# Kernel tuning notes

Hardware: AMD Instinct MI355X
Metric: run time of the kernel (lower is better)

The kernel has to match this reference:

```python
import jax, jax.numpy as jnp
import numpy as np

N_NODES = 100000
N_EDGES = 1600000
NODE_DIM = 128
EDGE_DIM = 32
HIDDEN_DIM = 256


def _linear_params(key, fan_in, fan_out):
    kw, kb = jax.random.split(key)
    bound = 1.0 / np.sqrt(fan_in)
    W = jax.random.uniform(kw, (fan_in, fan_out), minval=-bound, maxval=bound, dtype=jnp.float32)
    b = jax.random.uniform(kb, (fan_out,), minval=-bound, maxval=bound, dtype=jnp.float32)
    return W, b


def setup_inputs() -> dict:
    key = jax.random.key(0)
    ks = jax.random.split(key, 8)
    x = jax.random.normal(ks[0], (N_NODES, NODE_DIM), dtype=jnp.float32)
    edge_index = jax.random.randint(ks[1], (2, N_EDGES), 0, N_NODES, dtype=jnp.int64)
    edge_attr = jax.random.normal(ks[2], (N_EDGES, EDGE_DIM), dtype=jnp.float32)
    congestion = jax.random.uniform(ks[3], (N_NODES,), dtype=jnp.float32)
    msg_in = 2 * NODE_DIM + EDGE_DIM + 1
    mW1, mb1 = _linear_params(ks[4], msg_in, HIDDEN_DIM)
    mW2, mb2 = _linear_params(ks[5], HIDDEN_DIM, NODE_DIM)
    uW1, ub1 = _linear_params(ks[6], 2 * NODE_DIM, HIDDEN_DIM)
    uW2, ub2 = _linear_params(ks[7], HIDDEN_DIM, NODE_DIM)
    return {
        "x": x, "edge_index": edge_index, "edge_attr": edge_attr, "congestion": congestion,
        "mW1": mW1, "mb1": mb1, "mW2": mW2, "mb2": mb2,
        "uW1": uW1, "ub1": ub1, "uW2": uW2, "ub2": ub2,
    }


def reference(x, edge_index, edge_attr, congestion, mW1, mb1, mW2, mb2, uW1, ub1, uW2, ub2):
    src, dst = edge_index[0], edge_index[1]
    # gather node features and src congestion, concat along feature dim  [E, 2D+edge_dim+1]
    msg_in = jnp.concatenate(
        [x[src], x[dst], edge_attr, congestion[src][:, None]], axis=-1)
    h = jax.nn.relu(msg_in @ mW1 + mb1)          # [E, hidden]
    messages = h @ mW2 + mb2                     # [E, node_dim]
    # scatter_add messages into destination nodes  [N, node_dim]
    aggregated = jax.ops.segment_sum(messages, dst, num_segments=x.shape[0])
    upd_in = jnp.concatenate([x, aggregated], axis=-1)  # [N, 2*node_dim]
    h2 = jax.nn.relu(upd_in @ uW1 + ub1)
    x_new = h2 @ uW2 + ub2                       # [N, node_dim]
    return x_new
```

## Files before the change

### kernel.cpp

```cpp
#include <hip/hip_runtime.h>

#define E_TOTAL 1600000
#define NN 100000
#define D 128
#define ED 32
#define H 256

typedef __attribute__((ext_vector_type(8))) short s16x8;
typedef __attribute__((ext_vector_type(4))) short s16x4;
typedef __attribute__((ext_vector_type(4))) float f32x4;

#define MFMA(a, b, c) __builtin_amdgcn_mfma_f32_16x16x32_bf16((a), (b), (c), 0, 0, 0)

__device__ __forceinline__ short f2bf(float f) {
    unsigned u = __builtin_bit_cast(unsigned, f);
    u += 0x7fffu + ((u >> 16) & 1u);
    return (short)(u >> 16);
}

__device__ __forceinline__ void gll16(const void* g, void* l) {
    __builtin_amdgcn_global_load_lds(
        (const __attribute__((address_space(1))) void*)g,
        (__attribute__((address_space(3))) void*)l, 16, 0, 0);
}

__global__ void k_cvt_x(const float* __restrict__ x, short* __restrict__ xb, int n) {
    int i = (blockIdx.x * blockDim.x + threadIdx.x) * 4;
    if (i >= n) return;
    f32x4 v = *(const f32x4*)(x + i);
    s16x4 o;
    o[0] = f2bf(v[0]); o[1] = f2bf(v[1]); o[2] = f2bf(v[2]); o[3] = f2bf(v[3]);
    *(s16x4*)(xb + i) = o;
}

__global__ void k_swz(const float* __restrict__ W, short* __restrict__ out,
                      int K, int N, int total) {
    int idx = blockIdx.x * blockDim.x + threadIdx.x;
    if (idx >= total) return;
    int j    = idx & 7;
    int lane = (idx >> 3) & 63;
    int rest = idx >> 9;
    int NT   = N >> 4;
    int nt   = rest % NT;
    int t    = rest / NT;
    int k    = t * 32 + (lane >> 4) * 8 + j;
    int col  = nt * 16 + (lane & 15);
    float v  = (k < K) ? W[k * N + col] : 0.f;
    out[idx] = f2bf(v);
}

__global__ void k_hist(const int* __restrict__ ei, int* __restrict__ cnt) {
    int e = blockIdx.x * blockDim.x + threadIdx.x;
    if (e >= E_TOTAL) return;
    atomicAdd(&cnt[ei[E_TOTAL + e]], 1);
}

__global__ void k_scan1(int* __restrict__ cnt, int* __restrict__ psum, int n) {
    __shared__ int wsum[16];
    __shared__ int woff[16];
    const int tid = threadIdx.x, lane = tid & 63, wv = tid >> 6;
    int i = blockIdx.x * 1024 + tid;
    int v = (i < n) ? cnt[i] : 0;
    int s = v;
#pragma unroll
    for (int off = 1; off < 64; off <<= 1) {
        int u = __shfl_up(s, off, 64);
        if (lane >= off) s += u;
    }
    if (lane == 63) wsum[wv] = s;
    __syncthreads();
    if (wv == 0 && lane < 16) {
        int t = wsum[lane];
        int sc = t;
#pragma unroll
        for (int off = 1; off < 16; off <<= 1) {
            int u = __shfl_up(sc, off, 16);
            if (lane >= off) sc += u;
        }
        woff[lane] = sc - t;
    }
    __syncthreads();
    int excl = (s - v) + woff[wv];
    if (i < n) cnt[i] = excl;
    if (tid == 1023) psum[blockIdx.x] = excl + v;
}

__global__ void k_scan2(int* __restrict__ psum, int nb) {
    __shared__ int w0;
    const int tid = threadIdx.x, lane = tid & 63, wv = tid >> 6;
    int v = (tid < nb) ? psum[tid] : 0;
    int s = v;
#pragma unroll
    for (int off = 1; off < 64; off <<= 1) {
        int u = __shfl_up(s, off, 64);
        if (lane >= off) s += u;
    }
    if (wv == 0 && lane == 63) w0 = s;
    __syncthreads();
    int excl = (s - v) + (wv ? w0 : 0);
    if (tid < nb) psum[tid] = excl;
}

__global__ void k_scan3(const int* __restrict__ psum, int* __restrict__ cnt, int n) {
    int i = blockIdx.x * 1024 + threadIdx.x;
    if (i < n) cnt[i] += psum[blockIdx.x];
}

__global__ void k_perm(const int* __restrict__ ei, int* __restrict__ cursor,
                       int* __restrict__ perm, int2* __restrict__ srcdst) {
    int e = blockIdx.x * blockDim.x + threadIdx.x;
    if (e >= E_TOTAL) return;
    int s = ei[e], d = ei[E_TOTAL + e];
    int pos = atomicAdd(&cursor[d], 1);
    perm[pos] = e;
    srcdst[pos] = make_int2(s, d);
}

__global__ __launch_bounds__(512, 4)
void k_edge(const short* __restrict__ xb, const int* __restrict__ perm,
            const int2* __restrict__ srcdst,
            const float* __restrict__ eattr, const float* __restrict__ cong,
            const short* __restrict__ W1s, const float* __restrict__ b1,
            const short* __restrict__ W2s, const float* __restrict__ b2,
            float* __restrict__ agg) {
    __shared__ char smem[73728];
    __shared__ int   dst_s[128];
    __shared__ short cong_s[128];

    const int tid  = threadIdx.x;
    const int lane = tid & 63;
    const int w    = tid >> 6;
    const int eh   = w >> 2;
    const int cg   = w & 3;
    const int m    = lane & 15;
    const int q    = lane >> 4;
    const int p0b  = blockIdx.x * 128;

    {
        int edge = w * 16 + (lane >> 2);
        int2 sd  = srcdst[p0b + edge];
        int kqs  = (lane & 3) ^ ((lane >> 3) & 3);
        const char* gx0 = (const char*)xb + (long)sd.x * 256 + kqs * 16;
        const char* gx1 = (const char*)xb + (long)sd.y * 256 + kqs * 16;
#pragma unroll
        for (int t = 0; t < 4; t++)
            gll16(gx0 + t * 64, smem + t * 8192 + w * 1024);
#pragma unroll
        for (int t = 0; t < 4; t++)
            gll16(gx1 + t * 64, smem + (4 + t) * 8192 + w * 1024);
        int ea = perm[p0b + edge];
        const float* ge = eattr + (long)ea * ED + kqs * 8;
        f32x4 e0 = *(const f32x4*)ge, e1 = *(const f32x4*)(ge + 4);
        s16x8 ev;
#pragma unroll
        for (int j = 0; j < 4; j++) { ev[j] = f2bf(e0[j]); ev[4 + j] = f2bf(e1[j]); }
        *(s16x8*)(smem + 8 * 8192 + w * 1024 + lane * 16) = ev;
        if (tid < 128) {
            int2 sd2 = srcdst[p0b + tid];
            dst_s[tid]  = sd2.y;
            cong_s[tid] = f2bf(cong[sd2.x]);
        }
    }
    __syncthreads();

    const int rdoff = m * 64 + ((q ^ ((m >> 1) & 3)) << 4);

    f32x4 acc[4][4];
#pragma unroll
    for (int mt = 0; mt < 4; mt++)
#pragma unroll
        for (int n = 0; n < 4; n++) acc[mt][n] = (f32x4){0.f, 0.f, 0.f, 0.f};

#pragma unroll
    for (int t = 0; t < 9; t++) {
        s16x8 b[4];
        const short* bw = W1s + (t * 16 + cg * 4) * 512 + lane * 8;
#pragma unroll
        for (int n = 0; n < 4; n++) b[n] = *(const s16x8*)(bw + n * 512);
#pragma unroll
        for (int mt = 0; mt < 4; mt++) {
            s16x8 a = *(const s16x8*)(smem + t * 8192 + (eh * 4 + mt) * 1024 + rdoff);
#pragma unroll
            for (int n = 0; n < 4; n++) acc[mt][n] = MFMA(a, b[n], acc[mt][n]);
        }
    }
    {
        s16x8 b[4];
        const short* bw = W1s + (9 * 16 + cg * 4) * 512 + lane * 8;
#pragma unroll
        for (int n = 0; n < 4; n++) b[n] = *(const s16x8*)(bw + n * 512);
#pragma unroll
        for (int mt = 0; mt < 4; mt++) {
            s16x8 a = (s16x8){0, 0, 0, 0, 0, 0, 0, 0};
            short cv = cong_s[eh * 64 + mt * 16 + m];
            a[0] = (q == 0) ? cv : (short)0;
#pragma unroll
            for (int n = 0; n < 4; n++) acc[mt][n] = MFMA(a, b[n], acc[mt][n]);
        }
    }
    __syncthreads();

    {
        short* hb16 = (short*)smem;
#pragma unroll
        for (int n = 0; n < 4; n++) {
            const int chunk = 2 * cg + (n >> 1);
            const int srq   = (n & 1) * 2 + (m >> 3);
            const float bias = b1[cg * 64 + n * 16 + m];
#pragma unroll
            for (int mt = 0; mt < 4; mt++) {
#pragma unroll
                for (int r = 0; r < 4; r++) {
                    int edge = eh * 64 + mt * 16 + q * 4 + r;
                    int key  = (2 * q + (r >> 1)) & 3;
                    int phys = srq ^ key;
                    float v  = acc[mt][n][r] + bias;
                    hb16[chunk * 4096 + edge * 32 + phys * 8 + (m & 7)] =
                        f2bf(v > 0.f ? v : 0.f);
                }
            }
        }
    }
    __syncthreads();

    f32x4 acc2[4][2];
#pragma unroll
    for (int mt = 0; mt < 4; mt++) {
        acc2[mt][0] = (f32x4){0.f, 0.f, 0.f, 0.f};
        acc2[mt][1] = (f32x4){0.f, 0.f, 0.f, 0.f};
    }
#pragma unroll
    for (int t2 = 0; t2 < 8; t2++) {
        const short* bw = W2s + (t2 * 8 + cg * 2) * 512 + lane * 8;
        s16x8 b0  = *(const s16x8*)bw;
        s16x8 b1v = *(const s16x8*)(bw + 512);
#pragma unroll
        for (int mt = 0; mt < 4; mt++) {
            s16x8 a = *(const s16x8*)(smem + t2 * 8192 + (eh * 4 + mt) * 1024 + rdoff);
            acc2[mt][0] = MFMA(a, b0, acc2[mt][0]);
            acc2[mt][1] = MFMA(a, b1v, acc2[mt][1]);
        }
    }
    __syncthreads();

    {
        float (*mbuf)[132] = (float (*)[132])smem;
        float bb0 = b2[cg * 32 + m];
        float bb1 = b2[cg * 32 + 16 + m];
#pragma unroll
        for (int mt = 0; mt < 4; mt++)
#pragma unroll
            for (int r = 0; r < 4; r++) {
                int edge = eh * 64 + mt * 16 + q * 4 + r;
                mbuf[edge][cg * 32 + m]      = acc2[mt][0][r] + bb0;
                mbuf[edge][cg * 32 + 16 + m] = acc2[mt][1][r] + bb1;
            }
    }
    __syncthreads();

    {
        float (*mbuf)[132] = (float (*)[132])smem;
        const int qtr = tid >> 7, cc = tid & 127;
        float s = 0.f;
        int prev = dst_s[qtr * 32];
        for (int row = qtr * 32; row < qtr * 32 + 32; row++) {
            int dcur = dst_s[row];
            if (dcur != prev) {
                __hip_atomic_fetch_add(agg + (long)prev * D + cc, s,
                                       __ATOMIC_RELAXED, __HIP_MEMORY_SCOPE_AGENT);
                s = 0.f; prev = dcur;
            }
            s += mbuf[row][cc];
        }
        __hip_atomic_fetch_add(agg + (long)prev * D + cc, s,
                               __ATOMIC_RELAXED, __HIP_MEMORY_SCOPE_AGENT);
    }
}

__global__ __launch_bounds__(512, 4)
void k_node(const short* __restrict__ xb, const float* __restrict__ agg,
            const short* __restrict__ U1s, const float* __restrict__ b1,
            const short* __restrict__ U2s, const float* __restrict__ b2,
            float* __restrict__ out) {
    __shared__ char smem[65536];
    const int tid  = threadIdx.x;
    const int lane = tid & 63;
    const int w    = tid >> 6;
    const int eh   = w >> 2;
    const int cg   = w & 3;
    const int m    = lane & 15;
    const int q    = lane >> 4;
    const int r0   = blockIdx.x * 128;

    {
        int rowl = w * 16 + (lane >> 2);
        int grow = r0 + rowl;
        int gc   = grow < NN ? grow : 0;
        int kqs  = (lane & 3) ^ ((lane >> 3) & 3);
        const char* gx = (const char*)xb + (long)gc * 256 + kqs * 16;
#pragma unroll
        for (int t = 0; t < 4; t++)
            gll16(gx + t * 64, smem + t * 8192 + w * 1024);
        const float* ga = agg + (long)gc * D + kqs * 8;
#pragma unroll
        for (int t = 0; t < 4; t++) {
            f32x4 a0 = *(const f32x4*)(ga + t * 32);
            f32x4 a1 = *(const f32x4*)(ga + t * 32 + 4);
            s16x8 v;
#pragma unroll
            for (int j = 0; j < 4; j++) { v[j] = f2bf(a0[j]); v[4 + j] = f2bf(a1[j]); }
            *(s16x8*)(smem + (4 + t) * 8192 + w * 1024 + lane * 16) = v;
        }
    }
    __syncthreads();

    const int rdoff = m * 64 + ((q ^ ((m >> 1) & 3)) << 4);

    f32x4 acc[4][4];
#pragma unroll
    for (int mt = 0; mt < 4; mt++)
#pragma unroll
        for (int n = 0; n < 4; n++) acc[mt][n] = (f32x4){0.f, 0.f, 0.f, 0.f};

#pragma unroll
    for (int t = 0; t < 8; t++) {
        s16x8 b[4];
        const short* bw = U1s + (t * 16 + cg * 4) * 512 + lane * 8;
#pragma unroll
        for (int n = 0; n < 4; n++) b[n] = *(const s16x8*)(bw + n * 512);
#pragma unroll
        for (int mt = 0; mt < 4; mt++) {
            s16x8 a = *(const s16x8*)(smem + t * 8192 + (eh * 4 + mt) * 1024 + rdoff);
#pragma unroll
            for (int n = 0; n < 4; n++) acc[mt][n] = MFMA(a, b[n], acc[mt][n]);
        }
    }
    __syncthreads();

    {
        short* hb16 = (short*)smem;
#pragma unroll
        for (int n = 0; n < 4; n++) {
            const int chunk = 2 * cg + (n >> 1);
            const int srq   = (n & 1) * 2 + (m >> 3);
            const float bias = b1[cg * 64 + n * 16 + m];
#pragma unroll
            for (int mt = 0; mt < 4; mt++) {
#pragma unroll
                for (int r = 0; r < 4; r++) {
                    int row = eh * 64 + mt * 16 + q * 4 + r;
                    int key = (2 * q + (r >> 1)) & 3;
                    int phys = srq ^ key;
                    float v = acc[mt][n][r] + bias;
                    hb16[chunk * 4096 + row * 32 + phys * 8 + (m & 7)] =
                        f2bf(v > 0.f ? v : 0.f);
                }
            }
        }
    }
    __syncthreads();

    f32x4 acc2[4][2];
#pragma unroll
    for (int mt = 0; mt < 4; mt++) {
        acc2[mt][0] = (f32x4){0.f, 0.f, 0.f, 0.f};
        acc2[mt][1] = (f32x4){0.f, 0.f, 0.f, 0.f};
    }
#pragma unroll
    for (int t2 = 0; t2 < 8; t2++) {
        const short* bw = U2s + (t2 * 8 + cg * 2) * 512 + lane * 8;
        s16x8 b0  = *(const s16x8*)bw;
        s16x8 b1v = *(const s16x8*)(bw + 512);
#pragma unroll
        for (int mt = 0; mt < 4; mt++) {
            s16x8 a = *(const s16x8*)(smem + t2 * 8192 + (eh * 4 + mt) * 1024 + rdoff);
            acc2[mt][0] = MFMA(a, b0, acc2[mt][0]);
            acc2[mt][1] = MFMA(a, b1v, acc2[mt][1]);
        }
    }

    {
        float bb0 = b2[cg * 32 + m];
        float bb1 = b2[cg * 32 + 16 + m];
#pragma unroll
        for (int mt = 0; mt < 4; mt++)
#pragma unroll
            for (int r = 0; r < 4; r++) {
                int grow = r0 + eh * 64 + mt * 16 + q * 4 + r;
                if (grow < NN) {
                    out[(long)grow * D + cg * 32 + m]      = acc2[mt][0][r] + bb0;
                    out[(long)grow * D + cg * 32 + 16 + m] = acc2[mt][1][r] + bb1;
                }
            }
    }
}

extern "C" void kernel_launch(void* const* d_in, const int* in_sizes, int n_in,
                              void* d_out, int out_size, void* d_ws, size_t ws_size,
                              hipStream_t stream) {
    const float* x     = (const float*)d_in[0];
    const int*   ei    = (const int*)d_in[1];
    const float* eattr = (const float*)d_in[2];
    const float* cong  = (const float*)d_in[3];
    const float* mW1   = (const float*)d_in[4];
    const float* mb1   = (const float*)d_in[5];
    const float* mW2   = (const float*)d_in[6];
    const float* mb2   = (const float*)d_in[7];
    const float* uW1   = (const float*)d_in[8];
    const float* ub1   = (const float*)d_in[9];
    const float* uW2   = (const float*)d_in[10];
    const float* ub2   = (const float*)d_in[11];

    char* ws = (char*)d_ws;
    float* agg    = (float*)ws;
    short* xb     = (short*)(ws + 51200000);
    short* W1s    = (short*)(ws + 76800000);
    short* W2s    = (short*)(ws + 76963840);
    short* U1s    = (short*)(ws + 77029376);
    short* U2s    = (short*)(ws + 77160448);
    int*   cnt    = (int*)(ws + 77225984);
    int*   perm   = (int*)(ws + 77625984);
    int2*  srcdst = (int2*)(ws + 84025984);
    int*   psum   = (int*)(ws + 96825984);

    hipMemsetAsync(agg, 0, (size_t)NN * D * sizeof(float), stream);
    hipMemsetAsync(cnt, 0, (size_t)NN * sizeof(int), stream);

    k_cvt_x<<<(NN * D / 4 + 255) / 256, 256, 0, stream>>>(x, xb, NN * D);

    int tW1 = 10 * 16 * 512, tW2 = 8 * 8 * 512, tU1 = 8 * 16 * 512, tU2 = 8 * 8 * 512;
    k_swz<<<(tW1 + 255) / 256, 256, 0, stream>>>(mW1, W1s, 289, 256, tW1);
    k_swz<<<(tW2 + 255) / 256, 256, 0, stream>>>(mW2, W2s, 256, 128, tW2);
    k_swz<<<(tU1 + 255) / 256, 256, 0, stream>>>(uW1, U1s, 256, 256, tU1);
    k_swz<<<(tU2 + 255) / 256, 256, 0, stream>>>(uW2, U2s, 256, 128, tU2);

    int nb = (NN + 1023) / 1024;
    k_hist<<<(E_TOTAL + 255) / 256, 256, 0, stream>>>(ei, cnt);
    k_scan1<<<nb, 1024, 0, stream>>>(cnt, psum, NN);
    k_scan2<<<1, 128, 0, stream>>>(psum, nb);
    k_scan3<<<nb, 1024, 0, stream>>>(psum, cnt, NN);
    k_perm<<<(E_TOTAL + 255) / 256, 256, 0, stream>>>(ei, cnt, perm, srcdst);

    k_edge<<<E_TOTAL / 128, 512, 0, stream>>>(xb, perm, srcdst, eattr, cong,
                                              W1s, mb1, W2s, mb2, agg);
    k_node<<<(NN + 127) / 128, 512, 0, stream>>>(xb, agg, U1s, ub1, U2s, ub2,
                                                 (float*)d_out);
}
```

Measured before the change: 935.5 us.

## Precompute per-node dst projection of W1 and fuse prep kernels

Splits the first edge-MLP matmul by linearity. The x[dst] @ W1[128:256] term is computed once per node in a new kernel and stored as bf16. The edge kernel then gathers that row per edge instead of loading x[dst] and running four K-tiles of MFMAs, which cuts edge-side compute and LDS use. The conversion, histogram and weight-swizzle kernels are also merged into one launch. The cost is an extra 100k x 256 bf16 buffer, per-edge gathers of it, and a second bf16 rounding of the partial sum.

```diff
diff --git a/kernel.cpp b/kernel.cpp
--- a/kernel.cpp
+++ b/kernel.cpp
@@ -17,6 +17,9 @@
     u += 0x7fffu + ((u >> 16) & 1u);
     return (short)(u >> 16);
 }
+__device__ __forceinline__ float bf2f(short s) {
+    return __builtin_bit_cast(float, ((unsigned)(unsigned short)s) << 16);
+}
 
 __device__ __forceinline__ void gll16(const void* g, void* l) {
     __builtin_amdgcn_global_load_lds(
@@ -24,19 +27,9 @@
         (__attribute__((address_space(3))) void*)l, 16, 0, 0);
 }
 
-__global__ void k_cvt_x(const float* __restrict__ x, short* __restrict__ xb, int n) {
-    int i = (blockIdx.x * blockDim.x + threadIdx.x) * 4;
-    if (i >= n) return;
-    f32x4 v = *(const f32x4*)(x + i);
-    s16x4 o;
-    o[0] = f2bf(v[0]); o[1] = f2bf(v[1]); o[2] = f2bf(v[2]); o[3] = f2bf(v[3]);
-    *(s16x4*)(xb + i) = o;
-}
-
-__global__ void k_swz(const float* __restrict__ W, short* __restrict__ out,
-                      int K, int N, int total) {
-    int idx = blockIdx.x * blockDim.x + threadIdx.x;
-    if (idx >= total) return;
+__device__ __forceinline__ void swz_one(const float* __restrict__ W,
+                                        short* __restrict__ out,
+                                        int K, int N, int idx) {
     int j    = idx & 7;
     int lane = (idx >> 3) & 63;
     int rest = idx >> 9;
@@ -45,14 +38,36 @@
     int t    = rest / NT;
     int k    = t * 32 + (lane >> 4) * 8 + j;
     int col  = nt * 16 + (lane & 15);
-    float v  = (k < K) ? W[k * N + col] : 0.f;
-    out[idx] = f2bf(v);
-}
-
-__global__ void k_hist(const int* __restrict__ ei, int* __restrict__ cnt) {
-    int e = blockIdx.x * blockDim.x + threadIdx.x;
-    if (e >= E_TOTAL) return;
-    atomicAdd(&cnt[ei[E_TOTAL + e]], 1);
+    out[idx] = f2bf((k < K) ? W[k * N + col] : 0.f);
+}
+
+__global__ void k_prep(const float* __restrict__ x, short* __restrict__ xb,
+                       const int* __restrict__ ei, int* __restrict__ cnt,
+                       const float* __restrict__ mW1, short* __restrict__ W1s,
+                       const float* __restrict__ mW2, short* __restrict__ W2s,
+                       const float* __restrict__ uW1, short* __restrict__ U1s,
+                       const float* __restrict__ uW2, short* __restrict__ U2s) {
+    const int b = blockIdx.x;
+    if (b < 12500) {
+        int i = (b * 256 + threadIdx.x) * 4;
+        if (i >= NN * D) return;
+        f32x4 v = *(const f32x4*)(x + i);
+        s16x4 o;
+        o[0] = f2bf(v[0]); o[1] = f2bf(v[1]); o[2] = f2bf(v[2]); o[3] = f2bf(v[3]);
+        *(s16x4*)(xb + i) = o;
+    } else if (b < 18750) {
+        int e = (b - 12500) * 256 + threadIdx.x;
+        if (e < E_TOTAL) atomicAdd(&cnt[ei[E_TOTAL + e]], 1);
+    } else {
+        int idx = (b - 18750) * 256 + threadIdx.x;
+        if (idx < 81920) { swz_one(mW1, W1s, 289, 256, idx); return; }
+        idx -= 81920;
+        if (idx < 32768) { swz_one(mW2, W2s, 256, 128, idx); return; }
+        idx -= 32768;
+        if (idx < 65536) { swz_one(uW1, U1s, 256, 256, idx); return; }
+        idx -= 65536;
+        if (idx < 32768) { swz_one(uW2, U2s, 256, 128, idx); }
+    }
 }
 
 __global__ void k_scan1(int* __restrict__ cnt, int* __restrict__ psum, int n) {
@@ -117,13 +132,73 @@
 }
 
 __global__ __launch_bounds__(512, 4)
+void k_pre(const short* __restrict__ xb, const short* __restrict__ W1s,
+           short* __restrict__ yd) {
+    __shared__ char smem[32768];
+    const int tid  = threadIdx.x;
+    const int lane = tid & 63;
+    const int w    = tid >> 6;
+    const int eh   = w >> 2;
+    const int cg   = w & 3;
+    const int m    = lane & 15;
+    const int q    = lane >> 4;
+    const int r0   = blockIdx.x * 128;
+
+    {
+        int rowl = w * 16 + (lane >> 2);
+        int grow = r0 + rowl;
+        int gc   = grow < NN ? grow : 0;
+        int kqs  = (lane & 3) ^ ((lane >> 3) & 3);
+        const char* gx = (const char*)xb + (long)gc * 256 + kqs * 16;
+#pragma unroll
+        for (int t = 0; t < 4; t++)
+            gll16(gx + t * 64, smem + t * 8192 + w * 1024);
+    }
+    __syncthreads();
+
+    const int rdoff = m * 64 + ((q ^ ((m >> 1) & 3)) << 4);
+
+    f32x4 acc[4][4];
+#pragma unroll
+    for (int mt = 0; mt < 4; mt++)
+#pragma unroll
+        for (int n = 0; n < 4; n++) acc[mt][n] = (f32x4){0.f, 0.f, 0.f, 0.f};
+
+#pragma unroll
+    for (int t = 0; t < 4; t++) {
+        s16x8 b[4];
+        const short* bw = W1s + ((4 + t) * 16 + cg * 4) * 512 + lane * 8;
+#pragma unroll
+        for (int n = 0; n < 4; n++) b[n] = *(const s16x8*)(bw + n * 512);
+#pragma unroll
+        for (int mt = 0; mt < 4; mt++) {
+            s16x8 a = *(const s16x8*)(smem + t * 8192 + (eh * 4 + mt) * 1024 + rdoff);
+#pragma unroll
+            for (int n = 0; n < 4; n++) acc[mt][n] = MFMA(a, b[n], acc[mt][n]);
+        }
+    }
+
+#pragma unroll
+    for (int mt = 0; mt < 4; mt++)
+#pragma unroll
+        for (int r = 0; r < 4; r++) {
+            int grow = r0 + eh * 64 + mt * 16 + q * 4 + r;
+            if (grow < NN) {
+#pragma unroll
+                for (int n = 0; n < 4; n++)
+                    yd[(long)grow * H + cg * 64 + n * 16 + m] = f2bf(acc[mt][n][r]);
+            }
+        }
+}
+
+__global__ __launch_bounds__(512, 4)
 void k_edge(const short* __restrict__ xb, const int* __restrict__ perm,
-            const int2* __restrict__ srcdst,
+            const int2* __restrict__ srcdst, const short* __restrict__ yd,
             const float* __restrict__ eattr, const float* __restrict__ cong,
             const short* __restrict__ W1s, const float* __restrict__ b1,
             const short* __restrict__ W2s, const float* __restrict__ b2,
             float* __restrict__ agg) {
-    __shared__ char smem[73728];
+    __shared__ char smem[67584];
     __shared__ int   dst_s[128];
     __shared__ short cong_s[128];
 
@@ -141,20 +216,16 @@
         int2 sd  = srcdst[p0b + edge];
         int kqs  = (lane & 3) ^ ((lane >> 3) & 3);
         const char* gx0 = (const char*)xb + (long)sd.x * 256 + kqs * 16;
-        const char* gx1 = (const char*)xb + (long)sd.y * 256 + kqs * 16;
 #pragma unroll
         for (int t = 0; t < 4; t++)
             gll16(gx0 + t * 64, smem + t * 8192 + w * 1024);
-#pragma unroll
-        for (int t = 0; t < 4; t++)
-            gll16(gx1 + t * 64, smem + (4 + t) * 8192 + w * 1024);
         int ea = perm[p0b + edge];
         const float* ge = eattr + (long)ea * ED + kqs * 8;
         f32x4 e0 = *(const f32x4*)ge, e1 = *(const f32x4*)(ge + 4);
         s16x8 ev;
 #pragma unroll
         for (int j = 0; j < 4; j++) { ev[j] = f2bf(e0[j]); ev[4 + j] = f2bf(e1[j]); }
-        *(s16x8*)(smem + 8 * 8192 + w * 1024 + lane * 16) = ev;
+        *(s16x8*)(smem + 4 * 8192 + w * 1024 + lane * 16) = ev;
         if (tid < 128) {
             int2 sd2 = srcdst[p0b + tid];
             dst_s[tid]  = sd2.y;
@@ -172,9 +243,10 @@
         for (int n = 0; n < 4; n++) acc[mt][n] = (f32x4){0.f, 0.f, 0.f, 0.f};
 
 #pragma unroll
-    for (int t = 0; t < 9; t++) {
+    for (int t = 0; t < 5; t++) {
+        const int wt = (t < 4) ? t : 8;
         s16x8 b[4];
-        const short* bw = W1s + (t * 16 + cg * 4) * 512 + lane * 8;
+        const short* bw = W1s + (wt * 16 + cg * 4) * 512 + lane * 8;
 #pragma unroll
         for (int n = 0; n < 4; n++) b[n] = *(const s16x8*)(bw + n * 512);
 #pragma unroll
@@ -203,18 +275,19 @@
     {
         short* hb16 = (short*)smem;
 #pragma unroll
-        for (int n = 0; n < 4; n++) {
-            const int chunk = 2 * cg + (n >> 1);
-            const int srq   = (n & 1) * 2 + (m >> 3);
-            const float bias = b1[cg * 64 + n * 16 + m];
-#pragma unroll
-            for (int mt = 0; mt < 4; mt++) {
-#pragma unroll
-                for (int r = 0; r < 4; r++) {
-                    int edge = eh * 64 + mt * 16 + q * 4 + r;
-                    int key  = (2 * q + (r >> 1)) & 3;
+        for (int mt = 0; mt < 4; mt++) {
+#pragma unroll
+            for (int r = 0; r < 4; r++) {
+                int edge = eh * 64 + mt * 16 + q * 4 + r;
+                int key  = (2 * q + (r >> 1)) & 3;
+                const short* ydp = yd + (long)dst_s[edge] * H + cg * 64 + m;
+#pragma unroll
+                for (int n = 0; n < 4; n++) {
+                    const int chunk = 2 * cg + (n >> 1);
+                    const int srq   = (n & 1) * 2 + (m >> 3);
                     int phys = srq ^ key;
-                    float v  = acc[mt][n][r] + bias;
+                    float v  = acc[mt][n][r] + b1[cg * 64 + n * 16 + m]
+                             + bf2f(ydp[n * 16]);
                     hb16[chunk * 4096 + edge * 32 + phys * 8 + (m & 7)] =
                         f2bf(v > 0.f ? v : 0.f);
                 }
@@ -422,26 +495,23 @@
     int*   perm   = (int*)(ws + 77625984);
     int2*  srcdst = (int2*)(ws + 84025984);
     int*   psum   = (int*)(ws + 96825984);
+    short* yd     = (short*)(ws + 96826496);
 
     hipMemsetAsync(agg, 0, (size_t)NN * D * sizeof(float), stream);
     hipMemsetAsync(cnt, 0, (size_t)NN * sizeof(int), stream);
 
-    k_cvt_x<<<(NN * D / 4 + 255) / 256, 256, 0, stream>>>(x, xb, NN * D);
-
-    int tW1 = 10 * 16 * 512, tW2 = 8 * 8 * 512, tU1 = 8 * 16 * 512, tU2 = 8 * 8 * 512;
-    k_swz<<<(tW1 + 255) / 256, 256, 0, stream>>>(mW1, W1s, 289, 256, tW1);
-    k_swz<<<(tW2 + 255) / 256, 256, 0, stream>>>(mW2, W2s, 256, 128, tW2);
-    k_swz<<<(tU1 + 255) / 256, 256, 0, stream>>>(uW1, U1s, 256, 256, tU1);
-    k_swz<<<(tU2 + 255) / 256, 256, 0, stream>>>(uW2, U2s, 256, 128, tU2);
+    k_prep<<<19582, 256, 0, stream>>>(x, xb, ei, cnt,
+                                      mW1, W1s, mW2, W2s, uW1, U1s, uW2, U2s);
+
+    k_pre<<<(NN + 127) / 128, 512, 0, stream>>>(xb, W1s, yd);
 
     int nb = (NN + 1023) / 1024;
-    k_hist<<<(E_TOTAL + 255) / 256, 256, 0, stream>>>(ei, cnt);
     k_scan1<<<nb, 1024, 0, stream>>>(cnt, psum, NN);
     k_scan2<<<1, 128, 0, stream>>>(psum, nb);
     k_scan3<<<nb, 1024, 0, stream>>>(psum, cnt, NN);
     k_perm<<<(E_TOTAL + 255) / 256, 256, 0, stream>>>(ei, cnt, perm, srcdst);
 
-    k_edge<<<E_TOTAL / 128, 512, 0, stream>>>(xb, perm, srcdst, eattr, cong,
+    k_edge<<<E_TOTAL / 128, 512, 0, stream>>>(xb, perm, srcdst, yd, eattr, cong,
                                               W1s, mb1, W2s, mb2, agg);
     k_node<<<(NN + 127) / 128, 512, 0, stream>>>(xb, agg, U1s, ub1, U2s, ub2,
                                                  (float*)d_out);
```

New measurement: 1.047 ms. +11.9%, slower.
